# Performance work log

Measured on AMD Instinct MI355X. Metric: run time of the kernel, lower is better.

Reference implementation:

```python
import jax, jax.numpy as jnp
import numpy as np

B, M, F = 1024, 32, 256   # batch, attention parts, feature dim
BATCH_K = 4               # images per class group


def setup_inputs() -> dict:
    key = jax.random.key(0)
    x = jax.random.normal(key, (B, M, F), dtype=jnp.float32)
    return {"x": x}


def reference(x):
    b, m, f = x.shape
    k = BATCH_K
    # pairwise squared distances per part: d[i,j,m] = ||x[i,m] - x[j,m]||^2
    sq = jnp.sum(x * x, axis=-1)                    # [B, M]
    gram = jnp.einsum('imf,jmf->ijm', x, x)         # [B, B, M]
    d = sq[:, None, :] + sq[None, :, :] - 2.0 * gram

    idx = jnp.arange(b)
    groups = idx // k
    # homo: same group, unordered pairs i<j (original sums each pair once)
    homo_mask = (groups[:, None] == groups[None, :]) & (idx[:, None] < idx[None, :])
    # heter: anchor group strictly before other's group (j >= (g+1)*k)
    heter_mask = groups[:, None] < groups[None, :]

    loss_homo = jnp.sum(jnp.where(homo_mask[:, :, None], d, 0.0))
    loss_heter = jnp.sum(jnp.where(heter_mask[:, :, None],
                                   jnp.maximum(1.0 - d, 0.0), 0.0))

    return (2.0 * loss_homo / (b * (k - 1)),
            2.0 * loss_heter / (b * (b - k)))
```

## Files before the change

### kernel.cpp

```cpp
#include <hip/hip_runtime.h>
#include <stdint.h>


typedef __attribute__((ext_vector_type(4))) float f32x4;
typedef __attribute__((ext_vector_type(8))) short bf16x8;

#define XB_OFF    0u
#define SQ_OFF    16777216u
#define HOMO_OFF  16908288u
#define HETER_OFF 16941056u

#define AS1 __attribute__((address_space(1)))
#define AS3 __attribute__((address_space(3)))

__device__ __forceinline__ void async16(const void* g, void* l) {
  __builtin_amdgcn_global_load_lds((const AS1 unsigned int*)(uintptr_t)g,
                                   (AS3 unsigned int*)(uintptr_t)l, 16, 0, 0);
}

__device__ __forceinline__ unsigned short f2bf(float f) {
  union { float f; unsigned u; } v; v.f = f;
  return (unsigned short)((v.u + 0x7fffu + ((v.u >> 16) & 1u)) >> 16);
}

__global__ __launch_bounds__(256) void k_fused(const float* __restrict__ x,
                                               unsigned short* __restrict__ xb,
                                               float* __restrict__ sq,
                                               float* __restrict__ homo_part) {
  const int task = blockIdx.x * 4 + (threadIdx.x >> 6);
  const int lane = threadIdx.x & 63;
  const int g = task >> 5;
  const int m = task & 31;

  const float* base = x + ((size_t)(g * 4) * 32 + m) * 256 + lane * 4;
  float4 v[4];
  float sqv[4];
  #pragma unroll
  for (int a = 0; a < 4; ++a) {
    v[a] = *(const float4*)(base + a * 8192);
    float s = v[a].x * v[a].x + v[a].y * v[a].y + v[a].z * v[a].z + v[a].w * v[a].w;
    #pragma unroll
    for (int off = 32; off; off >>= 1) s += __shfl_xor(s, off, 64);
    sqv[a] = s;
    const int i = g * 4 + a;
    if (lane == 0) sq[m * 1024 + i] = s;
    ushort4 o;
    o.x = f2bf(v[a].x); o.y = f2bf(v[a].y); o.z = f2bf(v[a].z); o.w = f2bf(v[a].w);
    *(ushort4*)(xb + ((size_t)(m * 1024 + i)) * 256 + lane * 4) = o;
  }
  const float sx = v[0].x + v[1].x + v[2].x + v[3].x;
  const float sy = v[0].y + v[1].y + v[2].y + v[3].y;
  const float sz = v[0].z + v[1].z + v[2].z + v[3].z;
  const float sw = v[0].w + v[1].w + v[2].w + v[3].w;
  float s = sx * sx + sy * sy + sz * sz + sw * sw;
  #pragma unroll
  for (int off = 32; off; off >>= 1) s += __shfl_xor(s, off, 64);
  if (lane == 0)
    homo_part[task] = 4.f * (sqv[0] + sqv[1] + sqv[2] + sqv[3]) - s;
}

__device__ __forceinline__ void stage_panel(const unsigned short* __restrict__ X,
                                            int k0, unsigned short* buf, int tid) {
  #pragma unroll
  for (int i = 0; i < 2; ++i) {
    const int ch = i * 256 + tid;
    const int row = ch >> 2;
    const int c   = ch & 3;
    async16(X + (size_t)row * 256 + k0 + c * 8, (char*)buf + ch * 16);
  }
}

__global__ __launch_bounds__(256, 4) void k_heter(const unsigned short* __restrict__ xb,
                                                  const float* __restrict__ sq,
                                                  float* __restrict__ heter_part) {
  const int d = blockIdx.x;
  const int w = (d & 7) * 144 + (d >> 3);
  const int m = w / 36;
  int t0 = w - m * 36, r = 0;
  while (t0 >= 8 - r) { t0 -= 8 - r; ++r; }
  const int cb = r + t0;
  const bool diag = (cb == r);

  __shared__ __align__(16) unsigned short A0[4096], A1[4096];
  __shared__ __align__(16) unsigned short B0[4096], B1[4096];
  __shared__ __align__(16) float sql[1024];
  __shared__ float part[4];

  const int tid = threadIdx.x;
  const int lane = tid & 63;
  const int wid = tid >> 6;
  const int wr = wid >> 1, wc = wid & 1;
  const int fr = lane & 15;
  const int kg = lane >> 4;

  const unsigned short* Xa = xb + ((size_t)m * 1024 + r  * 128) * 256;
  const unsigned short* Xb = xb + ((size_t)m * 1024 + cb * 128) * 256;

  async16(sq + m * 1024 + tid * 4, (char*)sql + tid * 16);
  stage_panel(Xa, 0, A0, tid);
  if (!diag) stage_panel(Xb, 0, B0, tid);
  stage_panel(Xa, 32, A1, tid);
  if (!diag) stage_panel(Xb, 32, B1, tid);

  f32x4 acc[4][4] = {};

  #pragma unroll
  for (int s = 0; s < 8; ++s) {
    if (s < 7) {
      if (diag) asm volatile("s_waitcnt vmcnt(2)" ::: "memory");
      else      asm volatile("s_waitcnt vmcnt(4)" ::: "memory");
    } else {
      asm volatile("s_waitcnt vmcnt(0)" ::: "memory");
    }
    __builtin_amdgcn_s_barrier();
    asm volatile("" ::: "memory");

    const unsigned short* lA = (s & 1) ? A1 : A0;
    const unsigned short* lB = diag ? lA : ((s & 1) ? B1 : B0);
    bf16x8 af[4], bv[4];
    #pragma unroll
    for (int q = 0; q < 4; ++q) {
      const int ra = wr * 64 + q * 16 + fr;
      af[q] = *(const bf16x8*)(lA + ra * 32 + kg * 8);
      const int rb = wc * 64 + q * 16 + fr;
      bv[q] = *(const bf16x8*)(lB + rb * 32 + kg * 8);
    }
    #pragma unroll
    for (int ai = 0; ai < 4; ++ai)
      #pragma unroll
      for (int bj = 0; bj < 4; ++bj)
        acc[ai][bj] = __builtin_amdgcn_mfma_f32_16x16x32_bf16(af[ai], bv[bj],
                                                              acc[ai][bj], 0, 0, 0);

    asm volatile("" ::: "memory");
    __builtin_amdgcn_s_barrier();
    asm volatile("" ::: "memory");
    if (s + 2 < 8) {
      stage_panel(Xa, (s + 2) * 32, (s & 1) ? A1 : A0, tid);
      if (!diag) stage_panel(Xb, (s + 2) * 32, (s & 1) ? B1 : B0, tid);
    }
  }

  const int ibase = r  * 128 + wr * 64;
  const int jbase = cb * 128 + wc * 64;
  float sqi[4][4];
  #pragma unroll
  for (int ai = 0; ai < 4; ++ai)
    #pragma unroll
    for (int rg = 0; rg < 4; ++rg)
      sqi[ai][rg] = sql[ibase + ai * 16 + kg * 4 + rg];

  float local = 0.f;
  #pragma unroll
  for (int bj = 0; bj < 4; ++bj) {
    const int j = jbase + bj * 16 + fr;
    const float sqj = sql[j];
    const int gj = j >> 2;
    #pragma unroll
    for (int ai = 0; ai < 4; ++ai)
      #pragma unroll
      for (int rg = 0; rg < 4; ++rg) {
        const int i = ibase + ai * 16 + kg * 4 + rg;
        const float dd = sqi[ai][rg] + sqj - 2.f * acc[ai][bj][rg];
        const float v = 1.f - dd;
        if (v > 0.f && gj > (i >> 2)) local += v;
      }
  }
  #pragma unroll
  for (int off = 32; off; off >>= 1) local += __shfl_xor(local, off, 64);
  if (lane == 0) part[wid] = local;
  __syncthreads();
  if (tid == 0) heter_part[w] = part[0] + part[1] + part[2] + part[3];
}

__global__ __launch_bounds__(256) void k_final(const float* __restrict__ homo_part,
                                               const float* __restrict__ heter_part,
                                               float* __restrict__ out) {
  __shared__ float red[8];
  const int tid = threadIdx.x;
  const int lane = tid & 63;
  const int wid = tid >> 6;

  float h = 0.f;
  for (int i = tid; i < 8192; i += 256) h += homo_part[i];
  #pragma unroll
  for (int off = 32; off; off >>= 1) h += __shfl_xor(h, off, 64);
  if (lane == 0) red[wid] = h;

  float e = 0.f;
  for (int i = tid; i < 1152; i += 256) e += heter_part[i];
  #pragma unroll
  for (int off = 32; off; off >>= 1) e += __shfl_xor(e, off, 64);
  if (lane == 0) red[4 + wid] = e;

  __syncthreads();
  if (tid == 0) out[0] = (red[0] + red[1] + red[2] + red[3]) * (1.0f / 1536.0f);
  if (tid == 1) out[1] = (red[4] + red[5] + red[6] + red[7]) * (1.0f / 522240.0f);
}

extern "C" void kernel_launch(void* const* d_in, const int* in_sizes, int n_in,
                              void* d_out, int out_size, void* d_ws, size_t ws_size,
                              hipStream_t stream) {
  const float* x = (const float*)d_in[0];
  float* out = (float*)d_out;
  char* ws = (char*)d_ws;
  unsigned short* xb = (unsigned short*)(ws + XB_OFF);
  float* sq         = (float*)(ws + SQ_OFF);
  float* homo_part  = (float*)(ws + HOMO_OFF);
  float* heter_part = (float*)(ws + HETER_OFF);

  k_fused<<<2048, 256, 0, stream>>>(x, xb, sq, homo_part);
  k_heter<<<1152, 256, 0, stream>>>(xb, sq, heter_part);
  k_final<<<1, 256, 0, stream>>>(homo_part, heter_part, out);
}
```

Baseline: 38.36 us.

## Give each wave a private LDS tile pipeline, swizzled and barrier-free

The heter GEMM kernel now gives each wave its own 64x64 sub-tile with private double-buffered LDS staging, so the per-step block-wide barriers go away and waves advance independently. The LDS chunk order is XOR-swizzled to cut bank conflicts, and the lower-left wave on diagonal tiles is skipped because it holds no valid pairs. Diagonal waves on the main diagonal share their A and B panels, and sq is now read straight from global memory. The cost is duplicated global loads, since A and B panels are no longer shared across waves, plus 64KB LDS per block, which lowers occupancy.

```diff
diff --git a/kernel.cpp b/kernel.cpp
--- a/kernel.cpp
+++ b/kernel.cpp
@@ -59,20 +59,20 @@
     homo_part[task] = 4.f * (sqv[0] + sqv[1] + sqv[2] + sqv[3]) - s;
 }
 
-__device__ __forceinline__ void stage_panel(const unsigned short* __restrict__ X,
-                                            int k0, unsigned short* buf, int tid) {
-  #pragma unroll
-  for (int i = 0; i < 2; ++i) {
-    const int ch = i * 256 + tid;
+__device__ __forceinline__ void stage_wtile(const unsigned short* __restrict__ G,
+                                            int k0, char* buf, int lane) {
+  #pragma unroll
+  for (int i = 0; i < 4; ++i) {
+    const int ch = i * 64 + lane;
     const int row = ch >> 2;
-    const int c   = ch & 3;
-    async16(X + (size_t)row * 256 + k0 + c * 8, (char*)buf + ch * 16);
+    const int gc = (ch & 3) ^ ((row >> 1) & 3);
+    async16(G + (size_t)row * 256 + k0 + gc * 8, buf + ch * 16);
   }
 }
 
-__global__ __launch_bounds__(256, 4) void k_heter(const unsigned short* __restrict__ xb,
-                                                  const float* __restrict__ sq,
-                                                  float* __restrict__ heter_part) {
+__global__ __launch_bounds__(256) void k_heter(const unsigned short* __restrict__ xb,
+                                               const float* __restrict__ sq,
+                                               float* __restrict__ heter_part) {
   const int d = blockIdx.x;
   const int w = (d & 7) * 144 + (d >> 3);
   const int m = w / 36;
@@ -81,9 +81,7 @@
   const int cb = r + t0;
   const bool diag = (cb == r);
 
-  __shared__ __align__(16) unsigned short A0[4096], A1[4096];
-  __shared__ __align__(16) unsigned short B0[4096], B1[4096];
-  __shared__ __align__(16) float sql[1024];
+  __shared__ __align__(16) char lds[65536];
   __shared__ float part[4];
 
   const int tid = threadIdx.x;
@@ -93,81 +91,83 @@
   const int fr = lane & 15;
   const int kg = lane >> 4;
 
-  const unsigned short* Xa = xb + ((size_t)m * 1024 + r  * 128) * 256;
-  const unsigned short* Xb = xb + ((size_t)m * 1024 + cb * 128) * 256;
-
-  async16(sq + m * 1024 + tid * 4, (char*)sql + tid * 16);
-  stage_panel(Xa, 0, A0, tid);
-  if (!diag) stage_panel(Xb, 0, B0, tid);
-  stage_panel(Xa, 32, A1, tid);
-  if (!diag) stage_panel(Xb, 32, B1, tid);
-
-  f32x4 acc[4][4] = {};
-
-  #pragma unroll
-  for (int s = 0; s < 8; ++s) {
-    if (s < 7) {
-      if (diag) asm volatile("s_waitcnt vmcnt(2)" ::: "memory");
-      else      asm volatile("s_waitcnt vmcnt(4)" ::: "memory");
-    } else {
-      asm volatile("s_waitcnt vmcnt(0)" ::: "memory");
+  float local = 0.f;
+  const bool skip = diag && wr == 1 && wc == 0;
+
+  if (!skip) {
+    const bool share = diag && (wr == wc);
+    const unsigned short* Ag = xb + ((size_t)m * 1024 + r  * 128 + wr * 64) * 256;
+    const unsigned short* Bg = xb + ((size_t)m * 1024 + cb * 128 + wc * 64) * 256;
+    char* const base = lds + wid * 16384;
+    char* const A0 = base, * const B0 = base + 4096;
+    char* const A1 = base + 8192, * const B1 = base + 12288;
+
+    stage_wtile(Ag, 0, A0, lane);
+    if (!share) stage_wtile(Bg, 0, B0, lane);
+    stage_wtile(Ag, 32, A1, lane);
+    if (!share) stage_wtile(Bg, 32, B1, lane);
+
+    const int rch = (kg ^ ((fr >> 1) & 3)) << 4;
+    f32x4 acc[4][4] = {};
+
+    #pragma unroll
+    for (int s = 0; s < 8; ++s) {
+      if (s < 7) {
+        if (share) asm volatile("s_waitcnt vmcnt(4)" ::: "memory");
+        else       asm volatile("s_waitcnt vmcnt(8)" ::: "memory");
+      } else {
+        asm volatile("s_waitcnt vmcnt(0)" ::: "memory");
+      }
+      const char* lA = (s & 1) ? A1 : A0;
+      const char* lB = share ? lA : ((s & 1) ? B1 : B0);
+      bf16x8 af[4], bv[4];
+      #pragma unroll
+      for (int q = 0; q < 4; ++q) {
+        const int rloc = q * 16 + fr;
+        af[q] = *(const bf16x8*)(lA + rloc * 64 + rch);
+        bv[q] = *(const bf16x8*)(lB + rloc * 64 + rch);
+      }
+      #pragma unroll
+      for (int ai = 0; ai < 4; ++ai)
+        #pragma unroll
+        for (int bj = 0; bj < 4; ++bj)
+          acc[ai][bj] = __builtin_amdgcn_mfma_f32_16x16x32_bf16(af[ai], bv[bj],
+                                                                acc[ai][bj], 0, 0, 0);
+      asm volatile("s_waitcnt lgkmcnt(0)" ::: "memory");
+      if (s + 2 < 8) {
+        stage_wtile(Ag, (s + 2) * 32, (s & 1) ? A1 : A0, lane);
+        if (!share) stage_wtile(Bg, (s + 2) * 32, (s & 1) ? B1 : B0, lane);
+      }
     }
-    __builtin_amdgcn_s_barrier();
-    asm volatile("" ::: "memory");
-
-    const unsigned short* lA = (s & 1) ? A1 : A0;
-    const unsigned short* lB = diag ? lA : ((s & 1) ? B1 : B0);
-    bf16x8 af[4], bv[4];
-    #pragma unroll
-    for (int q = 0; q < 4; ++q) {
-      const int ra = wr * 64 + q * 16 + fr;
-      af[q] = *(const bf16x8*)(lA + ra * 32 + kg * 8);
-      const int rb = wc * 64 + q * 16 + fr;
-      bv[q] = *(const bf16x8*)(lB + rb * 32 + kg * 8);
+
+    const int ibase = r  * 128 + wr * 64;
+    const int jbase = cb * 128 + wc * 64;
+    const float* sqm = sq + m * 1024;
+    float sqi[4][4];
+    #pragma unroll
+    for (int ai = 0; ai < 4; ++ai)
+      #pragma unroll
+      for (int rg = 0; rg < 4; ++rg)
+        sqi[ai][rg] = sqm[ibase + ai * 16 + kg * 4 + rg];
+    #pragma unroll
+    for (int bj = 0; bj < 4; ++bj) {
+      const int j = jbase + bj * 16 + fr;
+      const float sqj = sqm[j];
+      const int gj = j >> 2;
+      #pragma unroll
+      for (int ai = 0; ai < 4; ++ai)
+        #pragma unroll
+        for (int rg = 0; rg < 4; ++rg) {
+          const int i = ibase + ai * 16 + kg * 4 + rg;
+          const float dd = sqi[ai][rg] + sqj - 2.f * acc[ai][bj][rg];
+          const float v = 1.f - dd;
+          if (v > 0.f && gj > (i >> 2)) local += v;
+        }
     }
     #pragma unroll
-    for (int ai = 0; ai < 4; ++ai)
-      #pragma unroll
-      for (int bj = 0; bj < 4; ++bj)
-        acc[ai][bj] = __builtin_amdgcn_mfma_f32_16x16x32_bf16(af[ai], bv[bj],
-                                                              acc[ai][bj], 0, 0, 0);
-
-    asm volatile("" ::: "memory");
-    __builtin_amdgcn_s_barrier();
-    asm volatile("" ::: "memory");
-    if (s + 2 < 8) {
-      stage_panel(Xa, (s + 2) * 32, (s & 1) ? A1 : A0, tid);
-      if (!diag) stage_panel(Xb, (s + 2) * 32, (s & 1) ? B1 : B0, tid);
-    }
+    for (int off = 32; off; off >>= 1) local += __shfl_xor(local, off, 64);
   }
 
-  const int ibase = r  * 128 + wr * 64;
-  const int jbase = cb * 128 + wc * 64;
-  float sqi[4][4];
-  #pragma unroll
-  for (int ai = 0; ai < 4; ++ai)
-    #pragma unroll
-    for (int rg = 0; rg < 4; ++rg)
-      sqi[ai][rg] = sql[ibase + ai * 16 + kg * 4 + rg];
-
-  float local = 0.f;
-  #pragma unroll
-  for (int bj = 0; bj < 4; ++bj) {
-    const int j = jbase + bj * 16 + fr;
-    const float sqj = sql[j];
-    const int gj = j >> 2;
-    #pragma unroll
-    for (int ai = 0; ai < 4; ++ai)
-      #pragma unroll
-      for (int rg = 0; rg < 4; ++rg) {
-        const int i = ibase + ai * 16 + kg * 4 + rg;
-        const float dd = sqi[ai][rg] + sqj - 2.f * acc[ai][bj][rg];
-        const float v = 1.f - dd;
-        if (v > 0.f && gj > (i >> 2)) local += v;
-      }
-  }
-  #pragma unroll
-  for (int off = 32; off; off >>= 1) local += __shfl_xor(local, off, 64);
   if (lane == 0) part[wid] = local;
   __syncthreads();
   if (tid == 0) heter_part[w] = part[0] + part[1] + part[2] + part[3];
```

New measurement: 42.04 us. 9.6% more time.
